# Performance work log

Hardware: AMD Instinct MI355X
Metric: run time of the kernel (lower is better)

Reference implementation:

```python
import jax, jax.numpy as jnp
import numpy as np

N_DET, N_T, NY, NX, B = 128, 2048, 256, 256, 4


def setup_inputs() -> dict:
    key = jax.random.key(0)
    k1, k2, k3 = jax.random.split(key, 3)
    sino = jax.random.normal(k1, (B, 1, N_DET, N_T), dtype=jnp.float32)
    # lut[..., 0]: fractional time-of-flight index in [0, n_t-1)
    tof = jax.random.uniform(k2, (NY, NX, N_DET), dtype=jnp.float32) * (N_T - 1)
    # lut[..., 1]: linear-interp fraction alpha in [0, 1)
    alpha = jax.random.uniform(k3, (NY, NX, N_DET), dtype=jnp.float32)
    lut = jnp.stack([tof, alpha], axis=-1)  # [ny, nx, n_det, 2]
    return {"sino": sino, "lut": lut}


def reference(sino, lut):
    b, _, n_det, n_t = sino.shape
    ny, nx = lut.shape[0], lut.shape[1]
    P = ny * nx

    # Precompute (as in __init__): floor index, validity mask, interp fraction.
    k_floor = jnp.floor(lut[..., 0])
    valid = (k_floor >= 0) & (k_floor < n_t - 1)
    k0 = jnp.clip(k_floor, 0, max(n_t - 2, 0)).astype(jnp.int32)  # [ny,nx,n_det]
    alpha = lut[..., 1]

    # Hann apodization window over detectors (non-trainable buffer).
    apod = (0.5 - 0.5 * jnp.cos(
        2.0 * jnp.pi * jnp.arange(n_det, dtype=jnp.float32) / max(n_det - 1, 1)
    )).astype(sino.dtype)

    S = sino[:, 0]  # [B, n_det, n_t]

    # Move detector axis first so we can gather all detectors at once.
    k0t = k0.reshape(P, n_det).T          # [n_det, P]
    at = alpha.reshape(P, n_det).T        # [n_det, P]
    vt = valid.reshape(P, n_det).T.astype(sino.dtype)  # [n_det, P]

    s0 = jnp.take_along_axis(S, k0t[None], axis=2)        # [B, n_det, P]
    s1 = jnp.take_along_axis(S, (k0t + 1)[None], axis=2)  # [B, n_det, P]
    sk = ((1.0 - at) * s0 + at * s1) * vt                  # masked lerp

    out = jnp.einsum('d,bdp->bp', apod, sk)                # apodized reduce over detectors
    norm = jnp.maximum(apod.sum(), jnp.finfo(apod.dtype).tiny)
    return (out / norm).reshape(b, 1, ny, nx)
```

## Files before the change

### kernel.cpp

```cpp
#include <hip/hip_runtime.h>

#define N_DET 128
#define N_T   2048
#define NPIX  65536
#define BATCH 4

__global__ __launch_bounds__(256) void sino_transpose_kernel(
    const float* __restrict__ sino, float* __restrict__ wsT) {
  int idx = blockIdx.x * blockDim.x + threadIdx.x;
  float4 v;
  v.x = sino[0 * N_DET * N_T + idx];
  v.y = sino[1 * N_DET * N_T + idx];
  v.z = sino[2 * N_DET * N_T + idx];
  v.w = sino[3 * N_DET * N_T + idx];
  reinterpret_cast<float4*>(wsT)[idx] = v;
}

template <bool TRANSPOSED>
__global__ __launch_bounds__(256) void das_kernel(
    const float* __restrict__ lut, const float* __restrict__ S,
    float* __restrict__ out) {
  const int lane = threadIdx.x & 63;
  const int p = blockIdx.x * 4 + (threadIdx.x >> 6);

  float4 lv = reinterpret_cast<const float4*>(lut + (size_t)p * 2 * N_DET)[lane];

  float acc0 = 0.f, acc1 = 0.f, acc2 = 0.f, acc3 = 0.f;
  float wsum = 0.f;

#pragma unroll
  for (int j = 0; j < 2; ++j) {
    const int d = 2 * lane + j;
    const float tof = j ? lv.z : lv.x;
    const float a   = j ? lv.w : lv.y;

    const float kf  = floorf(tof);
    const bool valid = (kf >= 0.0f) && (kf < (float)(N_T - 1));
    const float kcl = fminf(fmaxf(kf, 0.0f), (float)(N_T - 2));
    const int k0 = (int)kcl;

    const float apd =
        0.5f - 0.5f * cosf(6.28318530717958647692f * (1.0f / (float)(N_DET - 1)) * (float)d);
    wsum += apd;
    const float w = valid ? apd : 0.0f;
    const float om = 1.0f - a;

    if (TRANSPOSED) {
      const float4* row = reinterpret_cast<const float4*>(S) + (size_t)d * N_T;
      const float4 s0 = row[k0];
      const float4 s1 = row[k0 + 1];
      acc0 += w * (om * s0.x + a * s1.x);
      acc1 += w * (om * s0.y + a * s1.y);
      acc2 += w * (om * s0.z + a * s1.z);
      acc3 += w * (om * s0.w + a * s1.w);
    } else {
      const float* row = S + (size_t)d * N_T + k0;
      acc0 += w * (om * row[0 * N_DET * N_T] + a * row[0 * N_DET * N_T + 1]);
      acc1 += w * (om * row[1 * N_DET * N_T] + a * row[1 * N_DET * N_T + 1]);
      acc2 += w * (om * row[2 * N_DET * N_T] + a * row[2 * N_DET * N_T + 1]);
      acc3 += w * (om * row[3 * N_DET * N_T] + a * row[3 * N_DET * N_T + 1]);
    }
  }

#pragma unroll
  for (int off = 32; off > 0; off >>= 1) {
    acc0 += __shfl_xor(acc0, off);
    acc1 += __shfl_xor(acc1, off);
    acc2 += __shfl_xor(acc2, off);
    acc3 += __shfl_xor(acc3, off);
    wsum += __shfl_xor(wsum, off);
  }

  if (lane == 0) {
    const float inv = 1.0f / fmaxf(wsum, 1.17549435e-38f);
    out[0 * NPIX + p] = acc0 * inv;
    out[1 * NPIX + p] = acc1 * inv;
    out[2 * NPIX + p] = acc2 * inv;
    out[3 * NPIX + p] = acc3 * inv;
  }
}

extern "C" void kernel_launch(void* const* d_in, const int* in_sizes, int n_in,
                              void* d_out, int out_size, void* d_ws, size_t ws_size,
                              hipStream_t stream) {
  const float* sino = (const float*)d_in[0];
  const float* lut  = (const float*)d_in[1];
  float* out = (float*)d_out;

  const size_t need = (size_t)N_DET * N_T * BATCH * sizeof(float);
  if (ws_size >= need) {
    float* wsT = (float*)d_ws;
    sino_transpose_kernel<<<(N_DET * N_T) / 256, 256, 0, stream>>>(sino, wsT);
    das_kernel<true><<<NPIX / 4, 256, 0, stream>>>(lut, wsT, out);
  } else {
    das_kernel<false><<<NPIX / 4, 256, 0, stream>>>(lut, sino, out);
  }
}
```

Baseline: 148.7 us.

## Pack sinogram into fp16 pairs so each gather needs one 16-byte load

The pre-pass now converts the sinogram to half precision and stores, for each (detector, time) entry, both the sample at t and at t+1 for all four batches in one 16-byte record. The main kernel then does a single float4 gather per detector instead of two, cutting random-access traffic. The cost is fp16 rounding of the input samples, which loosens accuracy against the fp32 reference, plus a slightly heavier pack kernel.

```diff
diff --git a/kernel.cpp b/kernel.cpp
--- a/kernel.cpp
+++ b/kernel.cpp
@@ -1,29 +1,33 @@
 #include <hip/hip_runtime.h>
+#include <hip/hip_fp16.h>
 
 #define N_DET 128
 #define N_T   2048
 #define NPIX  65536
-#define BATCH 4
+#define NBATCH 4
 
-__global__ __launch_bounds__(256) void sino_transpose_kernel(
-    const float* __restrict__ sino, float* __restrict__ wsT) {
-  int idx = blockIdx.x * blockDim.x + threadIdx.x;
-  float4 v;
-  v.x = sino[0 * N_DET * N_T + idx];
-  v.y = sino[1 * N_DET * N_T + idx];
-  v.z = sino[2 * N_DET * N_T + idx];
-  v.w = sino[3 * N_DET * N_T + idx];
-  reinterpret_cast<float4*>(wsT)[idx] = v;
+__global__ __launch_bounds__(256) void sino_pack_kernel(
+    const float* __restrict__ sino, float4* __restrict__ wsT) {
+  const int idx = blockIdx.x * blockDim.x + threadIdx.x;
+  const int t = idx & (N_T - 1);
+  const int idx1 = (t < N_T - 1) ? idx + 1 : idx;
+  __half h[8];
+#pragma unroll
+  for (int b = 0; b < NBATCH; ++b) {
+    h[b]     = __float2half(sino[b * N_DET * N_T + idx]);
+    h[b + 4] = __float2half(sino[b * N_DET * N_T + idx1]);
+  }
+  wsT[idx] = *reinterpret_cast<const float4*>(h);
 }
 
-template <bool TRANSPOSED>
-__global__ __launch_bounds__(256) void das_kernel(
-    const float* __restrict__ lut, const float* __restrict__ S,
+__global__ __launch_bounds__(256) void das_packed_kernel(
+    const float* __restrict__ lut, const float4* __restrict__ S,
     float* __restrict__ out) {
   const int lane = threadIdx.x & 63;
   const int p = blockIdx.x * 4 + (threadIdx.x >> 6);
 
-  float4 lv = reinterpret_cast<const float4*>(lut + (size_t)p * 2 * N_DET)[lane];
+  const float4 lv =
+      reinterpret_cast<const float4*>(lut + (size_t)p * 2 * N_DET)[lane];
 
   float acc0 = 0.f, acc1 = 0.f, acc2 = 0.f, acc3 = 0.f;
   float wsum = 0.f;
@@ -34,32 +38,81 @@
     const float tof = j ? lv.z : lv.x;
     const float a   = j ? lv.w : lv.y;
 
-    const float kf  = floorf(tof);
+    const float kf = floorf(tof);
     const bool valid = (kf >= 0.0f) && (kf < (float)(N_T - 1));
     const float kcl = fminf(fmaxf(kf, 0.0f), (float)(N_T - 2));
     const int k0 = (int)kcl;
 
     const float apd =
-        0.5f - 0.5f * cosf(6.28318530717958647692f * (1.0f / (float)(N_DET - 1)) * (float)d);
+        0.5f - 0.5f * cosf(6.28318530717958647692f *
+                           (1.0f / (float)(N_DET - 1)) * (float)d);
     wsum += apd;
     const float w = valid ? apd : 0.0f;
     const float om = 1.0f - a;
 
-    if (TRANSPOSED) {
-      const float4* row = reinterpret_cast<const float4*>(S) + (size_t)d * N_T;
-      const float4 s0 = row[k0];
-      const float4 s1 = row[k0 + 1];
-      acc0 += w * (om * s0.x + a * s1.x);
-      acc1 += w * (om * s0.y + a * s1.y);
-      acc2 += w * (om * s0.z + a * s1.z);
-      acc3 += w * (om * s0.w + a * s1.w);
-    } else {
-      const float* row = S + (size_t)d * N_T + k0;
-      acc0 += w * (om * row[0 * N_DET * N_T] + a * row[0 * N_DET * N_T + 1]);
-      acc1 += w * (om * row[1 * N_DET * N_T] + a * row[1 * N_DET * N_T + 1]);
-      acc2 += w * (om * row[2 * N_DET * N_T] + a * row[2 * N_DET * N_T + 1]);
-      acc3 += w * (om * row[3 * N_DET * N_T] + a * row[3 * N_DET * N_T + 1]);
-    }
+    const float4 v = S[(size_t)d * N_T + k0];
+    const __half2* hp = reinterpret_cast<const __half2*>(&v);
+    const float2 s0a = __half22float2(hp[0]);
+    const float2 s0b = __half22float2(hp[1]);
+    const float2 s1a = __half22float2(hp[2]);
+    const float2 s1b = __half22float2(hp[3]);
+
+    acc0 += w * (om * s0a.x + a * s1a.x);
+    acc1 += w * (om * s0a.y + a * s1a.y);
+    acc2 += w * (om * s0b.x + a * s1b.x);
+    acc3 += w * (om * s0b.y + a * s1b.y);
+  }
+
+#pragma unroll
+  for (int off = 32; off > 0; off >>= 1) {
+    acc0 += __shfl_xor(acc0, off);
+    acc1 += __shfl_xor(acc1, off);
+    acc2 += __shfl_xor(acc2, off);
+    acc3 += __shfl_xor(acc3, off);
+    wsum += __shfl_xor(wsum, off);
+  }
+
+  if (lane == 0) {
+    const float inv = 1.0f / fmaxf(wsum, 1.17549435e-38f);
+    out[0 * NPIX + p] = acc0 * inv;
+    out[1 * NPIX + p] = acc1 * inv;
+    out[2 * NPIX + p] = acc2 * inv;
+    out[3 * NPIX + p] = acc3 * inv;
+  }
+}
+
+__global__ __launch_bounds__(256) void das_fallback_kernel(
+    const float* __restrict__ lut, const float* __restrict__ S,
+    float* __restrict__ out) {
+  const int lane = threadIdx.x & 63;
+  const int p = blockIdx.x * 4 + (threadIdx.x >> 6);
+
+  const float4 lv =
+      reinterpret_cast<const float4*>(lut + (size_t)p * 2 * N_DET)[lane];
+
+  float acc0 = 0.f, acc1 = 0.f, acc2 = 0.f, acc3 = 0.f;
+  float wsum = 0.f;
+
+#pragma unroll
+  for (int j = 0; j < 2; ++j) {
+    const int d = 2 * lane + j;
+    const float tof = j ? lv.z : lv.x;
+    const float a   = j ? lv.w : lv.y;
+    const float kf = floorf(tof);
+    const bool valid = (kf >= 0.0f) && (kf < (float)(N_T - 1));
+    const float kcl = fminf(fmaxf(kf, 0.0f), (float)(N_T - 2));
+    const int k0 = (int)kcl;
+    const float apd =
+        0.5f - 0.5f * cosf(6.28318530717958647692f *
+                           (1.0f / (float)(N_DET - 1)) * (float)d);
+    wsum += apd;
+    const float w = valid ? apd : 0.0f;
+    const float om = 1.0f - a;
+    const float* row = S + (size_t)d * N_T + k0;
+    acc0 += w * (om * row[0 * N_DET * N_T] + a * row[0 * N_DET * N_T + 1]);
+    acc1 += w * (om * row[1 * N_DET * N_T] + a * row[1 * N_DET * N_T + 1]);
+    acc2 += w * (om * row[2 * N_DET * N_T] + a * row[2 * N_DET * N_T + 1]);
+    acc3 += w * (om * row[3 * N_DET * N_T] + a * row[3 * N_DET * N_T + 1]);
   }
 
 #pragma unroll
@@ -87,12 +140,12 @@
   const float* lut  = (const float*)d_in[1];
   float* out = (float*)d_out;
 
-  const size_t need = (size_t)N_DET * N_T * BATCH * sizeof(float);
+  const size_t need = (size_t)N_DET * N_T * sizeof(float4);
   if (ws_size >= need) {
-    float* wsT = (float*)d_ws;
-    sino_transpose_kernel<<<(N_DET * N_T) / 256, 256, 0, stream>>>(sino, wsT);
-    das_kernel<true><<<NPIX / 4, 256, 0, stream>>>(lut, wsT, out);
+    float4* wsT = (float4*)d_ws;
+    sino_pack_kernel<<<(N_DET * N_T) / 256, 256, 0, stream>>>(sino, wsT);
+    das_packed_kernel<<<NPIX / 4, 256, 0, stream>>>(lut, wsT, out);
   } else {
-    das_kernel<false><<<NPIX / 4, 256, 0, stream>>>(lut, sino, out);
+    das_fallback_kernel<<<NPIX / 4, 256, 0, stream>>>(lut, sino, out);
   }
 }
```

New measurement: 134.3 us. 1.11x faster.
